# Kernel tuning notes

Hardware: AMD Instinct MI355X
Metric: run time of the kernel (lower is better)

The kernel has to match this reference:

```python
import jax, jax.numpy as jnp
import numpy as np

B, S, D, H, HD = 2, 2048, 1024, 16, 64
SCALE = HD ** -0.5


def setup_inputs() -> dict:
    key = jax.random.key(0)
    ks = jax.random.split(key, 11)
    w = 0.02
    return {
        "query": jax.random.normal(ks[0], (B, S, D), jnp.float32),
        "key": jax.random.normal(ks[1], (B, S, D), jnp.float32),
        "value": jax.random.normal(ks[2], (B, S, D), jnp.float32),
        "Wq": jax.random.normal(ks[3], (D, H * HD), jnp.float32) * w,
        "bq": jnp.zeros((H * HD,), jnp.float32),
        "Wk": jax.random.normal(ks[4], (D, H * HD), jnp.float32) * w,
        "bk": jnp.zeros((H * HD,), jnp.float32),
        "Wv": jax.random.normal(ks[5], (D, H * HD), jnp.float32) * w,
        "bv": jnp.zeros((H * HD,), jnp.float32),
        "Wo": jax.random.normal(ks[6], (H * HD, D), jnp.float32) * w,
        "bo": jnp.zeros((D,), jnp.float32),
    }


def reference(query, key, value, Wq, bq, Wk, bk, Wv, bv, Wo, bo):
    # projections -> [B, H, S, HD]
    q = (query @ Wq + bq).reshape(B, S, H, HD).transpose(0, 2, 1, 3)
    k = (key @ Wk + bk).reshape(B, S, H, HD).transpose(0, 2, 1, 3)
    v = (value @ Wv + bv).reshape(B, S, H, HD).transpose(0, 2, 1, 3)
    # attention scores [B, H, S, S]
    attn_score = jnp.einsum("bhqd,bhkd->bhqk", q, k) * SCALE
    attn_weights = jax.nn.softmax(attn_score, axis=-1)
    out = jnp.einsum("bhqk,bhkd->bhqd", attn_weights, v)
    out = out.transpose(0, 2, 1, 3).reshape(B, S, H * HD)
    out = out @ Wo + bo
    return out, attn_weights
```

## Files before the change

kernel.cpp:

```cpp
#include <hip/hip_runtime.h>
#include <hip/hip_bf16.h>
#include <stdint.h>

#define B_ 2
#define S_ 2048
#define D_ 1024
#define H_ 16
#define HD_ 64
#define SCALE_ 0.125f
#define SC2_ 0.18033688011112042f

typedef __attribute__((ext_vector_type(8))) short bfx8;
typedef __attribute__((ext_vector_type(4))) float f32x4;

#define VWAIT(n) asm volatile("s_waitcnt vmcnt(" #n ")" ::: "memory")

__device__ __forceinline__ void gld_lds16(const void* g, void* l) {
    __builtin_amdgcn_global_load_lds(
        (const __attribute__((address_space(1))) void*)g,
        (__attribute__((address_space(3))) void*)l, 16, 0, 0);
}

__global__ __launch_bounds__(256) void cast3_bf16(
    const float* __restrict__ a, const float* __restrict__ b, const float* __restrict__ c,
    __hip_bfloat16* __restrict__ oa, __hip_bfloat16* __restrict__ ob, __hip_bfloat16* __restrict__ oc)
{
    const float* src = blockIdx.y == 0 ? a : blockIdx.y == 1 ? b : c;
    __hip_bfloat16* dst = blockIdx.y == 0 ? oa : blockIdx.y == 1 ? ob : oc;
    const size_t i = ((size_t)blockIdx.x * 256 + threadIdx.x) * 4;
    float4 v = *(const float4*)(src + i);
    ushort4 u;
    __hip_bfloat16 t;
    t = __float2bfloat16(v.x); u.x = *(unsigned short*)&t;
    t = __float2bfloat16(v.y); u.y = *(unsigned short*)&t;
    t = __float2bfloat16(v.z); u.z = *(unsigned short*)&t;
    t = __float2bfloat16(v.w); u.w = *(unsigned short*)&t;
    *(ushort4*)(dst + i) = u;
}

__global__ __launch_bounds__(256) void transpose_cast_w(
    const float* __restrict__ w0, const float* __restrict__ w1,
    const float* __restrict__ w2, const float* __restrict__ w3,
    __hip_bfloat16* __restrict__ o0, __hip_bfloat16* __restrict__ o1,
    __hip_bfloat16* __restrict__ o2, __hip_bfloat16* __restrict__ o3)
{
    __shared__ float t[32][33];
    const int z = blockIdx.z;
    const float* W = z == 0 ? w0 : z == 1 ? w1 : z == 2 ? w2 : w3;
    __hip_bfloat16* Wt = z == 0 ? o0 : z == 1 ? o1 : z == 2 ? o2 : o3;
    const int bx = blockIdx.x * 32, by = blockIdx.y * 32;
    const int x = threadIdx.x, y = threadIdx.y;
#pragma unroll
    for (int i = 0; i < 32; i += 8)
        t[y + i][x] = W[(size_t)(by + y + i) * 1024 + bx + x];
    __syncthreads();
#pragma unroll
    for (int i = 0; i < 32; i += 8)
        Wt[(size_t)(bx + y + i) * 1024 + by + x] = __float2bfloat16(t[x][y + i]);
}

__global__ __launch_bounds__(256) void transpose_v(
    const __hip_bfloat16* __restrict__ vn,
    __hip_bfloat16* __restrict__ vtb)
{
    __shared__ unsigned int t[64][65];
    const int bh = blockIdx.y;
    const int st = blockIdx.x;
    const int tid = threadIdx.x, lane = tid & 63, w = tid >> 6;
    {
        const int sl = tid >> 2, c0 = (tid & 3) * 16;
        const ushort4* src = (const ushort4*)(vn + ((size_t)bh * S_ + st * 64 + sl) * 64 + c0);
        ushort4 a = src[0], b = src[1], c = src[2], d = src[3];
        unsigned short vals[16] = {a.x,a.y,a.z,a.w,b.x,b.y,b.z,b.w,
                                   c.x,c.y,c.z,c.w,d.x,d.y,d.z,d.w};
#pragma unroll
        for (int j = 0; j < 16; ++j) t[sl][c0 + j] = vals[j];
    }
    __syncthreads();
    const int sl2 = (lane & 31) * 2;
    const int dh  = (lane >> 5) * 8;
#pragma unroll
    for (int j = 0; j < 8; ++j) {
        const int d = w * 16 + dh + j;
        const unsigned int lo = t[sl2][d], hi = t[sl2 + 1][d];
        const unsigned int pk = (lo & 0xFFFFu) | (hi << 16);
        *(unsigned int*)(vtb + ((size_t)bh * HD_ + d) * S_ + st * 64 + sl2) = pk;
    }
}

__device__ __forceinline__ void gemm_body(
    const __hip_bfloat16* __restrict__ A,
    const __hip_bfloat16* __restrict__ Bt,
    const float* __restrict__ bias,
    void* __restrict__ Cout, int mode,
    __hip_bfloat16 (*As)[128 * 32], __hip_bfloat16 (*Bs)[128 * 32],
    int bm, int bn)
{
    constexpr int K = 1024, N = 1024;
    const int tid = threadIdx.x;
    const int wid = tid >> 6, lane = tid & 63;
    const int wm = (wid >> 1) * 64, wn = (wid & 1) * 64;

    f32x4 acc[4][4] = {};

    const int srow = lane >> 2;
    const int scol = (lane & 3) * 8;

    auto stage = [&](int kt, int buf) {
#pragma unroll
        for (int i = 0; i < 2; ++i) {
            const int rb = wid * 32 + i * 16;
            gld_lds16(A  + (size_t)(bm + rb + srow) * K + kt * 32 + scol, (char*)As[buf] + rb * 64);
            gld_lds16(Bt + (size_t)(bn + rb + srow) * K + kt * 32 + scol, (char*)Bs[buf] + rb * 64);
        }
    };

    stage(0, 0);
    __syncthreads();

    for (int kt = 0; kt < K / 32; ++kt) {
        const int cur = kt & 1;
        if (kt < K / 32 - 1) stage(kt + 1, cur ^ 1);
        bfx8 af[4], bf[4];
#pragma unroll
        for (int m = 0; m < 4; ++m)
            af[m] = *(const bfx8*)((const char*)As[cur] + (wm + m * 16 + (lane & 15)) * 64 + (lane >> 4) * 16);
#pragma unroll
        for (int n = 0; n < 4; ++n)
            bf[n] = *(const bfx8*)((const char*)Bs[cur] + (wn + n * 16 + (lane & 15)) * 64 + (lane >> 4) * 16);
        __builtin_amdgcn_s_setprio(1);
#pragma unroll
        for (int m = 0; m < 4; ++m)
#pragma unroll
            for (int n = 0; n < 4; ++n)
                acc[m][n] = __builtin_amdgcn_mfma_f32_16x16x32_bf16(af[m], bf[n], acc[m][n], 0, 0, 0);
        __builtin_amdgcn_s_setprio(0);
        __syncthreads();
    }

#pragma unroll
    for (int m = 0; m < 4; ++m) {
        const int row0 = bm + wm + m * 16 + ((lane >> 4) << 2);
#pragma unroll
        for (int n = 0; n < 4; ++n) {
            const int col = bn + wn + n * 16 + (lane & 15);
            const float bv = bias[col];
#pragma unroll
            for (int r = 0; r < 4; ++r) {
                const int i = row0 + r;
                const float v = acc[m][n][r] + bv;
                if (mode == 2) {
                    ((float*)Cout)[(size_t)i * N + col] = v;
                } else {
                    const int b = i >> 11, s = i & 2047, h = col >> 6, d = col & 63;
                    ((__hip_bfloat16*)Cout)[(((size_t)b * H_ + h) * S_ + s) * HD_ + d] = __float2bfloat16(v);
                }
            }
        }
    }
}

__global__ __launch_bounds__(256, 3) void gemm_qkv(
    const __hip_bfloat16* __restrict__ xq, const __hip_bfloat16* __restrict__ xk,
    const __hip_bfloat16* __restrict__ xv,
    const __hip_bfloat16* __restrict__ Wqt, const __hip_bfloat16* __restrict__ Wkt,
    const __hip_bfloat16* __restrict__ Wvt,
    const float* __restrict__ bq, const float* __restrict__ bk, const float* __restrict__ bv,
    __hip_bfloat16* __restrict__ qb, __hip_bfloat16* __restrict__ kbuf,
    __hip_bfloat16* __restrict__ vnb)
{
    __shared__ __align__(16) __hip_bfloat16 As[2][128 * 32];
    __shared__ __align__(16) __hip_bfloat16 Bs[2][128 * 32];
    const int z = blockIdx.z;
    const __hip_bfloat16* A  = z == 0 ? xq : z == 1 ? xk : xv;
    const __hip_bfloat16* Bt = z == 0 ? Wqt : z == 1 ? Wkt : Wvt;
    const float* bias        = z == 0 ? bq : z == 1 ? bk : bv;
    void* out                = z == 0 ? (void*)qb : z == 1 ? (void*)kbuf : (void*)vnb;
    gemm_body(A, Bt, bias, out, 0, As, Bs, blockIdx.x * 128, blockIdx.y * 128);
}

__global__ __launch_bounds__(256, 3) void gemm_wo(
    const __hip_bfloat16* __restrict__ A, const __hip_bfloat16* __restrict__ Bt,
    const float* __restrict__ bias, float* __restrict__ Cout)
{
    __shared__ __align__(16) __hip_bfloat16 As[2][128 * 32];
    __shared__ __align__(16) __hip_bfloat16 Bs[2][128 * 32];
    gemm_body(A, Bt, bias, (void*)Cout, 2, As, Bs, blockIdx.x * 128, blockIdx.y * 128);
}

__global__ __launch_bounds__(256, 4) void attn_fused(
    const __hip_bfloat16* __restrict__ qb,
    const __hip_bfloat16* __restrict__ kb,
    const __hip_bfloat16* __restrict__ vt,
    float* __restrict__ attnw,
    __hip_bfloat16* __restrict__ aout)
{
    __shared__ __align__(16) char lds_[40960];
    char* const ps_ = lds_ + 32768;

    const int wg  = blockIdx.x;
    const int lin = (wg & 7) * 128 + (wg >> 3);
    const int bh  = lin >> 5;
    const int qt  = lin & 31;

    const int tid = threadIdx.x, wid = tid >> 6, lane = tid & 63;
    const int qrow0 = qt * 64 + wid * 16;

    const char* kh = (const char*)(kb + (size_t)bh * S_ * HD_);
    const char* vh = (const char*)(vt + (size_t)bh * HD_ * S_);

    bfx8 qf[2];
#pragma unroll
    for (int kx = 0; kx < 2; ++kx)
        qf[kx] = *(const bfx8*)(qb + ((size_t)bh * S_ + qrow0 + (lane & 15)) * HD_
                                 + kx * 32 + (lane >> 4) * 8);

    const int sr = lane >> 3;
    const int sc = lane & 7;

    auto stage_k = [&](int kt, char* dst) {
#pragma unroll
        for (int i = 0; i < 2; ++i) {
            const int rb = wid * 16 + i * 8;
            const int row = rb + sr;
            const int colb = (sc * 16) ^ ((row & 7) << 4);
            gld_lds16(kh + (size_t)(kt * 64 + row) * 128 + colb, dst + rb * 128);
        }
    };
    auto stage_v = [&](int kt, char* dst) {
#pragma unroll
        for (int i = 0; i < 2; ++i) {
            const int rb = wid * 16 + i * 8;
            const int row = rb + sr;
            const int colb = (sc * 16) ^ ((row & 7) << 4);
            gld_lds16(vh + ((size_t)row * S_ + kt * 64) * 2 + colb, dst + rb * 128);
        }
    };

    float lsum = 0.f;
    stage_k(0, lds_);
    stage_k(1, lds_ + 8192);
    for (int kt = 0; kt < 32; ++kt) {
        if (kt < 30) {
            stage_k(kt + 2, lds_ + ((kt + 2) & 3) * 8192);
            VWAIT(4);
        } else if (kt == 30) { VWAIT(2); } else { VWAIT(0); }
        __builtin_amdgcn_sched_barrier(0);
        __builtin_amdgcn_s_barrier();

        const char* kbase = lds_ + (kt & 3) * 8192;
        f32x4 c[4] = {};
#pragma unroll
        for (int kx = 0; kx < 2; ++kx) {
            bfx8 bfv[4];
#pragma unroll
            for (int cf = 0; cf < 4; ++cf) {
                const int row = cf * 16 + (lane & 15);
                bfv[cf] = *(const bfx8*)(kbase + row * 128
                                          + ((kx * 64 + (lane >> 4) * 16) ^ ((row & 7) << 4)));
            }
            __builtin_amdgcn_s_setprio(1);
#pragma unroll
            for (int cf = 0; cf < 4; ++cf)
                c[cf] = __builtin_amdgcn_mfma_f32_16x16x32_bf16(bfv[cf], qf[kx], c[cf], 0, 0, 0);
            __builtin_amdgcn_s_setprio(0);
        }
#pragma unroll
        for (int cf = 0; cf < 4; ++cf)
            lsum += exp2f(c[cf][0] * SC2_) + exp2f(c[cf][1] * SC2_)
                  + exp2f(c[cf][2] * SC2_) + exp2f(c[cf][3] * SC2_);
    }
    float llog;
    {
        float s = lsum;
        s += __shfl_xor(s, 16);
        s += __shfl_xor(s, 32);
        llog = -__log2f(s);
    }

    f32x4 o[4] = {};
    stage_k(0, lds_);
    stage_v(0, lds_ + 16384);
    VWAIT(0);
    __builtin_amdgcn_s_barrier();
    for (int kt = 0; kt < 32; ++kt) {
        const int cur = kt & 1;
        const char* ksb = lds_ + cur * 8192;
        const char* vsb = lds_ + 16384 + cur * 8192;

        if (kt < 31) {
            stage_k(kt + 1, lds_ + (cur ^ 1) * 8192);
            stage_v(kt + 1, lds_ + 16384 + (cur ^ 1) * 8192);
        }

        f32x4 c[4] = {};
#pragma unroll
        for (int kx = 0; kx < 2; ++kx) {
            bfx8 bfv[4];
#pragma unroll
            for (int cf = 0; cf < 4; ++cf) {
                const int row = cf * 16 + (lane & 15);
                bfv[cf] = *(const bfx8*)(ksb + row * 128
                                          + ((kx * 64 + (lane >> 4) * 16) ^ ((row & 7) << 4)));
            }
            __builtin_amdgcn_s_setprio(1);
#pragma unroll
            for (int cf = 0; cf < 4; ++cf)
                c[cf] = __builtin_amdgcn_mfma_f32_16x16x32_bf16(bfv[cf], qf[kx], c[cf], 0, 0, 0);
            __builtin_amdgcn_s_setprio(0);
        }

        {
            const int q = lane & 15;
            char* const prow_base = ps_ + (wid * 16 + q) * 128;
            const int swz = (q & 7) << 4;
#pragma unroll
            for (int cf = 0; cf < 4; ++cf) {
                const int k0b = (cf * 16 + (lane >> 4) * 4) * 2;
                ushort4 pk;
                __hip_bfloat16 bb;
                bb = __float2bfloat16(exp2f(fmaf(c[cf][0], SC2_, llog))); pk.x = *(unsigned short*)&bb;
                bb = __float2bfloat16(exp2f(fmaf(c[cf][1], SC2_, llog))); pk.y = *(unsigned short*)&bb;
                bb = __float2bfloat16(exp2f(fmaf(c[cf][2], SC2_, llog))); pk.z = *(unsigned short*)&bb;
                bb = __float2bfloat16(exp2f(fmaf(c[cf][3], SC2_, llog))); pk.w = *(unsigned short*)&bb;
                *(ushort4*)(prow_base + (k0b ^ swz)) = pk;
            }
        }

#pragma unroll
        for (int rr = 0; rr < 4; ++rr) {
            const int p = wid * 16 + rr * 4 + (lane >> 4);
            const uint2 u = *(const uint2*)(ps_ + p * 128
                                            + (((lane & 15) * 8) ^ ((p & 7) << 4)));
            f32x4 f;
            f[0] = __uint_as_float(u.x << 16);
            f[1] = __uint_as_float(u.x & 0xFFFF0000u);
            f[2] = __uint_as_float(u.y << 16);
            f[3] = __uint_as_float(u.y & 0xFFFF0000u);
            __builtin_nontemporal_store(f,
                (f32x4*)(attnw + ((size_t)bh * S_ + qt * 64 + p) * S_ + kt * 64 + (lane & 15) * 4));
        }

#pragma unroll
        for (int kx = 0; kx < 2; ++kx) {
            bfx8 pf, vf[4];
            {
                const int prow = wid * 16 + (lane & 15);
                pf = *(const bfx8*)(ps_ + prow * 128
                                     + ((kx * 64 + (lane >> 4) * 16) ^ ((prow & 7) << 4)));
            }
#pragma unroll
            for (int df = 0; df < 4; ++df) {
                const int vrow = df * 16 + (lane & 15);
                vf[df] = *(const bfx8*)(vsb + vrow * 128
                                         + ((kx * 64 + (lane >> 4) * 16) ^ ((vrow & 7) << 4)));
            }
            __builtin_amdgcn_s_setprio(1);
#pragma unroll
            for (int df = 0; df < 4; ++df)
                o[df] = __builtin_amdgcn_mfma_f32_16x16x32_bf16(pf, vf[df], o[df], 0, 0, 0);
            __builtin_amdgcn_s_setprio(0);
        }

        if (kt < 31) {
            VWAIT(4);
            __builtin_amdgcn_sched_barrier(0);
            __builtin_amdgcn_s_barrier();
        }
    }

    const int b = bh >> 4, h = bh & 15;
#pragma unroll
    for (int r = 0; r < 4; ++r) {
        const int s = qrow0 + ((lane >> 4) << 2) + r;
#pragma unroll
        for (int df = 0; df < 4; ++df) {
            const int d = df * 16 + (lane & 15);
            aout[((size_t)b * S_ + s) * D_ + h * HD_ + d] = __float2bfloat16(o[df][r]);
        }
    }
}

extern "C" void kernel_launch(void* const* d_in, const int* in_sizes, int n_in,
                              void* d_out, int out_size, void* d_ws, size_t ws_size,
                              hipStream_t stream)
{
    (void)in_sizes; (void)n_in; (void)out_size; (void)ws_size;
    const float* query = (const float*)d_in[0];
    const float* key_  = (const float*)d_in[1];
    const float* value = (const float*)d_in[2];
    const float* Wq = (const float*)d_in[3];
    const float* bq = (const float*)d_in[4];
    const float* Wk = (const float*)d_in[5];
    const float* bk = (const float*)d_in[6];
    const float* Wv = (const float*)d_in[7];
    const float* bv = (const float*)d_in[8];
    const float* Wo = (const float*)d_in[9];
    const float* bo = (const float*)d_in[10];

    char* ws = (char*)d_ws;
    const size_t MB = 1u << 20;
    __hip_bfloat16* xq   = (__hip_bfloat16*)(ws + 0 * MB);
    __hip_bfloat16* xk   = (__hip_bfloat16*)(ws + 8 * MB);
    __hip_bfloat16* xv   = (__hip_bfloat16*)(ws + 16 * MB);
    __hip_bfloat16* Wqt  = (__hip_bfloat16*)(ws + 24 * MB);
    __hip_bfloat16* Wkt  = (__hip_bfloat16*)(ws + 26 * MB);
    __hip_bfloat16* Wvt  = (__hip_bfloat16*)(ws + 28 * MB);
    __hip_bfloat16* Wot  = (__hip_bfloat16*)(ws + 30 * MB);
    __hip_bfloat16* qb   = (__hip_bfloat16*)(ws + 32 * MB);
    __hip_bfloat16* kbuf = (__hip_bfloat16*)(ws + 40 * MB);
    __hip_bfloat16* vtb  = (__hip_bfloat16*)(ws + 48 * MB);
    __hip_bfloat16* vnb  = (__hip_bfloat16*)(ws + 56 * MB);
    __hip_bfloat16* aout = (__hip_bfloat16*)(ws + 56 * MB);

    float* outp  = (float*)d_out;
    float* attnw = outp + (size_t)B_ * S_ * D_;

    cast3_bf16<<<dim3(4096, 3), 256, 0, stream>>>(query, key_, value, xq, xk, xv);
    transpose_cast_w<<<dim3(32, 32, 4), dim3(32, 8), 0, stream>>>(Wq, Wk, Wv, Wo, Wqt, Wkt, Wvt, Wot);
    gemm_qkv<<<dim3(32, 8, 3), 256, 0, stream>>>(xq, xk, xv, Wqt, Wkt, Wvt, bq, bk, bv, qb, kbuf, vnb);
    transpose_v<<<dim3(32, 32), 256, 0, stream>>>(vnb, vtb);
    attn_fused<<<dim3(1024), 256, 0, stream>>>(qb, kbuf, vtb, attnw, aout);
    gemm_wo<<<dim3(32, 8), 256, 0, stream>>>(aout, Wot, bo, outp);
}
```

Baseline: 205.0 us.

## Merge input/weight prep kernels and retile output GEMM to 128x64

Merges the activation bf16 cast and the weight transpose-cast into one launch, with the work chosen by block index, to save a kernel launch. Replaces the shared gemm_body for the output projection with a dedicated 128x64-tile MFMA kernel, doubling the grid from 256 to 512 blocks so the CUs are better filled. The trade-off is less reuse per tile and more total loads of A. The prep kernel now contains a __syncthreads inside a block-uniform branch, which is safe.

Result: no change. 201.2 us, median of 2 (-1.9%).

```diff
diff --git a/kernel.cpp b/kernel.cpp
--- a/kernel.cpp
+++ b/kernel.cpp
@@ -21,42 +21,46 @@
         (__attribute__((address_space(3))) void*)l, 16, 0, 0);
 }
 
-__global__ __launch_bounds__(256) void cast3_bf16(
+__global__ __launch_bounds__(256) void prep(
     const float* __restrict__ a, const float* __restrict__ b, const float* __restrict__ c,
-    __hip_bfloat16* __restrict__ oa, __hip_bfloat16* __restrict__ ob, __hip_bfloat16* __restrict__ oc)
-{
-    const float* src = blockIdx.y == 0 ? a : blockIdx.y == 1 ? b : c;
-    __hip_bfloat16* dst = blockIdx.y == 0 ? oa : blockIdx.y == 1 ? ob : oc;
-    const size_t i = ((size_t)blockIdx.x * 256 + threadIdx.x) * 4;
-    float4 v = *(const float4*)(src + i);
-    ushort4 u;
-    __hip_bfloat16 t;
-    t = __float2bfloat16(v.x); u.x = *(unsigned short*)&t;
-    t = __float2bfloat16(v.y); u.y = *(unsigned short*)&t;
-    t = __float2bfloat16(v.z); u.z = *(unsigned short*)&t;
-    t = __float2bfloat16(v.w); u.w = *(unsigned short*)&t;
-    *(ushort4*)(dst + i) = u;
-}
-
-__global__ __launch_bounds__(256) void transpose_cast_w(
+    __hip_bfloat16* __restrict__ oa, __hip_bfloat16* __restrict__ ob, __hip_bfloat16* __restrict__ oc,
     const float* __restrict__ w0, const float* __restrict__ w1,
     const float* __restrict__ w2, const float* __restrict__ w3,
     __hip_bfloat16* __restrict__ o0, __hip_bfloat16* __restrict__ o1,
     __hip_bfloat16* __restrict__ o2, __hip_bfloat16* __restrict__ o3)
 {
     __shared__ float t[32][33];
-    const int z = blockIdx.z;
-    const float* W = z == 0 ? w0 : z == 1 ? w1 : z == 2 ? w2 : w3;
-    __hip_bfloat16* Wt = z == 0 ? o0 : z == 1 ? o1 : z == 2 ? o2 : o3;
-    const int bx = blockIdx.x * 32, by = blockIdx.y * 32;
-    const int x = threadIdx.x, y = threadIdx.y;
-#pragma unroll
-    for (int i = 0; i < 32; i += 8)
-        t[y + i][x] = W[(size_t)(by + y + i) * 1024 + bx + x];
-    __syncthreads();
-#pragma unroll
-    for (int i = 0; i < 32; i += 8)
-        Wt[(size_t)(bx + y + i) * 1024 + by + x] = __float2bfloat16(t[x][y + i]);
+    const int bid = blockIdx.x;
+    if (bid < 12288) {
+        const int which = bid >> 12;
+        const int xb = bid & 4095;
+        const float* src = which == 0 ? a : which == 1 ? b : c;
+        __hip_bfloat16* dst = which == 0 ? oa : which == 1 ? ob : oc;
+        const size_t i = ((size_t)xb * 256 + threadIdx.x) * 4;
+        float4 v = *(const float4*)(src + i);
+        ushort4 u;
+        __hip_bfloat16 tt;
+        tt = __float2bfloat16(v.x); u.x = *(unsigned short*)&tt;
+        tt = __float2bfloat16(v.y); u.y = *(unsigned short*)&tt;
+        tt = __float2bfloat16(v.z); u.z = *(unsigned short*)&tt;
+        tt = __float2bfloat16(v.w); u.w = *(unsigned short*)&tt;
+        *(ushort4*)(dst + i) = u;
+    } else {
+        const int tb = bid - 12288;
+        const int z = tb >> 10;
+        const int rem = tb & 1023;
+        const int bx = (rem & 31) * 32, by = (rem >> 5) * 32;
+        const float* W = z == 0 ? w0 : z == 1 ? w1 : z == 2 ? w2 : w3;
+        __hip_bfloat16* Wt = z == 0 ? o0 : z == 1 ? o1 : z == 2 ? o2 : o3;
+        const int x = threadIdx.x & 31, y = threadIdx.x >> 5;
+#pragma unroll
+        for (int i = 0; i < 32; i += 8)
+            t[y + i][x] = W[(size_t)(by + y + i) * 1024 + bx + x];
+        __syncthreads();
+#pragma unroll
+        for (int i = 0; i < 32; i += 8)
+            Wt[(size_t)(bx + y + i) * 1024 + by + x] = __float2bfloat16(t[x][y + i]);
+    }
 }
 
 __global__ __launch_bounds__(256) void transpose_v(
@@ -179,13 +183,68 @@
     gemm_body(A, Bt, bias, out, 0, As, Bs, blockIdx.x * 128, blockIdx.y * 128);
 }
 
-__global__ __launch_bounds__(256, 3) void gemm_wo(
+__global__ __launch_bounds__(256, 2) void gemm_wo(
     const __hip_bfloat16* __restrict__ A, const __hip_bfloat16* __restrict__ Bt,
     const float* __restrict__ bias, float* __restrict__ Cout)
 {
+    constexpr int K = 1024, N = 1024;
     __shared__ __align__(16) __hip_bfloat16 As[2][128 * 32];
-    __shared__ __align__(16) __hip_bfloat16 Bs[2][128 * 32];
-    gemm_body(A, Bt, bias, (void*)Cout, 2, As, Bs, blockIdx.x * 128, blockIdx.y * 128);
+    __shared__ __align__(16) __hip_bfloat16 Bs[2][64 * 32];
+    const int tid = threadIdx.x;
+    const int wid = tid >> 6, lane = tid & 63;
+    const int wm = (wid >> 1) * 64, wn = (wid & 1) * 32;
+    const int bm = blockIdx.x * 128, bn = blockIdx.y * 64;
+
+    f32x4 acc[4][2] = {};
+
+    const int srow = lane >> 2;
+    const int scol = (lane & 3) * 8;
+
+    auto stage = [&](int kt, int buf) {
+#pragma unroll
+        for (int i = 0; i < 2; ++i) {
+            const int rb = wid * 32 + i * 16;
+            gld_lds16(A + (size_t)(bm + rb + srow) * K + kt * 32 + scol, (char*)As[buf] + rb * 64);
+        }
+        const int rbB = wid * 16;
+        gld_lds16(Bt + (size_t)(bn + rbB + srow) * K + kt * 32 + scol, (char*)Bs[buf] + rbB * 64);
+    };
+
+    stage(0, 0);
+    __syncthreads();
+
+    for (int kt = 0; kt < K / 32; ++kt) {
+        const int cur = kt & 1;
+        if (kt < K / 32 - 1) stage(kt + 1, cur ^ 1);
+        bfx8 af[4], bf[2];
+#pragma unroll
+        for (int m = 0; m < 4; ++m)
+            af[m] = *(const bfx8*)((const char*)As[cur] + (wm + m * 16 + (lane & 15)) * 64 + (lane >> 4) * 16);
+#pragma unroll
+        for (int n = 0; n < 2; ++n)
+            bf[n] = *(const bfx8*)((const char*)Bs[cur] + (wn + n * 16 + (lane & 15)) * 64 + (lane >> 4) * 16);
+        __builtin_amdgcn_s_setprio(1);
+#pragma unroll
+        for (int m = 0; m < 4; ++m)
+#pragma unroll
+            for (int n = 0; n < 2; ++n)
+                acc[m][n] = __builtin_amdgcn_mfma_f32_16x16x32_bf16(af[m], bf[n], acc[m][n], 0, 0, 0);
+        __builtin_amdgcn_s_setprio(0);
+        __syncthreads();
+    }
+
+#pragma unroll
+    for (int m = 0; m < 4; ++m) {
+        const int row0 = bm + wm + m * 16 + ((lane >> 4) << 2);
+#pragma unroll
+        for (int n = 0; n < 2; ++n) {
+            const int col = bn + wn + n * 16 + (lane & 15);
+            const float bv = bias[col];
+#pragma unroll
+            for (int r = 0; r < 4; ++r)
+                Cout[(size_t)(row0 + r) * N + col] = acc[m][n][r] + bv;
+        }
+    }
 }
 
 __global__ __launch_bounds__(256, 4) void attn_fused(
@@ -416,10 +475,10 @@
     float* outp  = (float*)d_out;
     float* attnw = outp + (size_t)B_ * S_ * D_;
 
-    cast3_bf16<<<dim3(4096, 3), 256, 0, stream>>>(query, key_, value, xq, xk, xv);
-    transpose_cast_w<<<dim3(32, 32, 4), dim3(32, 8), 0, stream>>>(Wq, Wk, Wv, Wo, Wqt, Wkt, Wvt, Wot);
+    prep<<<dim3(16384), 256, 0, stream>>>(query, key_, value, xq, xk, xv,
+                                          Wq, Wk, Wv, Wo, Wqt, Wkt, Wvt, Wot);
     gemm_qkv<<<dim3(32, 8, 3), 256, 0, stream>>>(xq, xk, xv, Wqt, Wkt, Wvt, bq, bk, bv, qb, kbuf, vnb);
     transpose_v<<<dim3(32, 32), 256, 0, stream>>>(vnb, vtb);
     attn_fused<<<dim3(1024), 256, 0, stream>>>(qb, kbuf, vtb, attnw, aout);
-    gemm_wo<<<dim3(32, 8), 256, 0, stream>>>(aout, Wot, bo, outp);
-}
+    gemm_wo<<<dim3(32, 16), 256, 0, stream>>>(aout, Wot, bo, outp);
+}
```
